# Performance work log

Measured on AMD Instinct MI355X. Metric: run time of the kernel, lower is better.

Reference implementation:

```python
import jax, jax.numpy as jnp
import numpy as np

N = 8192
F_DIM = 512
H_DIM = 256


def _xavier(key, shape):
    fan_in, fan_out = shape
    limit = float(np.sqrt(6.0 / (fan_in + fan_out)))
    return jax.random.uniform(key, shape, jnp.float32, -limit, limit)


def setup_inputs() -> dict:
    key = jax.random.key(0)
    k1, k2, k3, k4, k5, k6, k7 = jax.random.split(key, 7)
    inp = {
        "input": jax.random.normal(k1, (N, F_DIM), jnp.float32),
        "wavelets": jax.random.normal(k2, (N, N), jnp.float32) / np.sqrt(N),
        "wavelets_inv": jax.random.normal(k3, (N, N), jnp.float32) / np.sqrt(N),
        "W1": _xavier(k4, (F_DIM, H_DIM)),
        "W2": _xavier(k5, (H_DIM, H_DIM)),
        "filter1": jax.random.uniform(k6, (N,), jnp.float32, 0.9, 1.1),
        "filter2": jax.random.uniform(k7, (N,), jnp.float32, 0.9, 1.1),
    }
    return inp


def _gwnn_layer(x, wavelets, wavelets_inv, weight, filt):
    # torch: wavelets @ diag(filt) @ (wavelets_inv @ (x @ W))
    # diag(filt) right-multiply == column-wise scale of wavelets (same math,
    # avoids the O(N^3) dense diag matmul).
    t = x @ weight                      # [N, C_out]
    s = wavelets_inv @ t                # [N, C_out] (spectral domain)
    return (wavelets * filt[None, :]) @ s  # [N, C_out]


def reference(input, wavelets, wavelets_inv, W1, W2, filter1, filter2):
    # eval mode: dropout is identity
    h1 = jax.nn.relu(_gwnn_layer(input, wavelets, wavelets_inv, W1, filter1))
    out = _gwnn_layer(h1, wavelets, wavelets_inv, W2, filter2)
    return out
```

## Files before the change

kernel.cpp:

```cpp
#include <hip/hip_runtime.h>
#include <hip/hip_bf16.h>

using f32x4 = __attribute__((ext_vector_type(4))) float;
using s16x8 = __attribute__((ext_vector_type(8))) short;

#define DEVFN static __device__ __forceinline__

static constexpr int NCOL = 256;
static constexpr int MROWS = 8192;
static constexpr int BM = 128;
static constexpr int BK = 64;
static constexpr int THREADS = 512;
static constexpr int NTILE = MROWS / BM;
static constexpr size_t PSLICE = (size_t)MROWS * NCOL;

DEVFN unsigned short f2bf(float f) {
  union { float f; unsigned u; } x; x.f = f;
  unsigned u = x.u;
  u += 0x7fffu + ((u >> 16) & 1u);
  return (unsigned short)(u >> 16);
}

DEVFN float bf2f(unsigned short u) {
  union { unsigned u; float f; } x; x.u = (unsigned)u << 16; return x.f;
}

DEVFN s16x8 pack8(f32x4 v0, f32x4 v1) {
  union { s16x8 v; __hip_bfloat162 h[4]; } pk;
  pk.h[0] = __float22bfloat162_rn(float2{v0[0], v0[1]});
  pk.h[1] = __float22bfloat162_rn(float2{v0[2], v0[3]});
  pk.h[2] = __float22bfloat162_rn(float2{v1[0], v1[1]});
  pk.h[3] = __float22bfloat162_rn(float2{v1[2], v1[3]});
  return pk.v;
}

DEVFN void async16(void* lds, const void* g) {
  __builtin_amdgcn_global_load_lds((const __attribute__((address_space(1))) unsigned*)g,
                                   (__attribute__((address_space(3))) unsigned*)lds,
                                   16, 0, 0);
}


template<int KS>
__global__ __launch_bounds__(THREADS, 2)
void gemm_b(const unsigned short* __restrict__ Ablk, int Kfull,
            const unsigned short* __restrict__ Bp8,
            unsigned short* __restrict__ Pout)
{
  __shared__ __align__(16) unsigned short As[2][2 * 4096];
  __shared__ __align__(16) unsigned short Bs[2][BK * NCOL];

  const int nwg = NTILE * KS, q = nwg / 8;
  const int logical = (blockIdx.x & 7) * q + (blockIdx.x >> 3);
  const int kh = logical / NTILE;
  const int tile = logical % NTILE;
  const int klen = Kfull / KS;
  const int nt = klen / BK;
  const int k0 = kh * klen;
  const int KT = Kfull >> 6;
  const int tid = threadIdx.x, lane = tid & 63;
  const int wm = (tid >> 6) >> 2;
  const int wn = (tid >> 6) & 3;
  const int lr = lane & 15, lg = lane >> 4;

  auto stage = [&](int buf, int t) {
    const unsigned short* asrc = Ablk + ((size_t)(2 * tile) * KT + (k0 >> 6) + t) * 4096 + tid * 8;
    async16(&As[buf][tid * 8], asrc);
    async16(&As[buf][4096 + tid * 8], asrc + (size_t)KT * 4096);
    const unsigned short* bsrc = Bp8 + (size_t)(k0 + t * BK) * NCOL + tid * 8;
#pragma unroll
    for (int o = 0; o < 4; ++o)
      async16(&Bs[buf][o * 4096 + tid * 8], bsrc + o * 4096);
  };

  f32x4 acc[4][4] = {};

  stage(0, 0);

  int cur = 0;
  for (int t = 0; t < nt; ++t) {
    if (t + 1 < nt) {
      stage(cur ^ 1, t + 1);
      asm volatile("s_waitcnt vmcnt(6)");
    } else {
      asm volatile("s_waitcnt vmcnt(0)");
    }
    __builtin_amdgcn_s_barrier();
    __builtin_amdgcn_sched_barrier(0);
#pragma unroll
    for (int s = 0; s < 2; ++s) {
      const int kc = s * 4 + lg;
      s16x8 af[4], bf[4];
#pragma unroll
      for (int fm = 0; fm < 4; ++fm) {
        const int ir = fm * 16 + lr;
        af[fm] = *(const s16x8*)&As[cur][wm * 4096 + ir * 64 + ((kc ^ (ir & 7)) << 3)];
      }
#pragma unroll
      for (int fn = 0; fn < 4; ++fn)
        bf[fn] = *(const s16x8*)&Bs[cur][kc * 2048 + (wn * 64 + fn * 16 + lr) * 8];
#pragma unroll
      for (int fm = 0; fm < 4; ++fm)
#pragma unroll
        for (int fn = 0; fn < 4; ++fn)
          acc[fm][fn] = __builtin_amdgcn_mfma_f32_16x16x32_bf16(af[fm], bf[fn], acc[fm][fn], 0, 0, 0);
    }
    __builtin_amdgcn_s_barrier();
    cur ^= 1;
  }

  unsigned short* dst = Pout + (size_t)kh * PSLICE;
#pragma unroll
  for (int fm = 0; fm < 4; ++fm) {
    const int r0 = tile * BM + wm * 64 + fm * 16 + lg * 4;
#pragma unroll
    for (int fn = 0; fn < 4; ++fn) {
      const int col = wn * 64 + fn * 16 + lr;
      ushort4 u;
      u.x = f2bf(acc[fm][fn][0]); u.y = f2bf(acc[fm][fn][1]);
      u.z = f2bf(acc[fm][fn][2]); u.w = f2bf(acc[fm][fn][3]);
      *(ushort4*)&dst[((size_t)(r0 >> 3) * 256 + col) * 8 + (r0 & 7)] = u;
    }
  }
}


template<int KTSH>
__global__ void k_cvt_ablk(const float* __restrict__ W, unsigned short* __restrict__ outp) {
  const int K = 64 << KTSH;
  size_t gid = (size_t)blockIdx.x * blockDim.x + threadIdx.x;
  const int k8 = (int)(gid & 7);
  const size_t rr = gid >> 3;
  const int row = (int)(rr & 63);
  const size_t bt = rr >> 6;
  const int t = (int)(bt & ((1 << KTSH) - 1));
  const size_t T = bt >> KTSH;
  const float* p = W + (T * 64 + row) * (size_t)K + t * 64 + k8 * 8;
  s16x8 v = pack8(*(const f32x4*)p, *(const f32x4*)(p + 4));
  *(s16x8*)&outp[bt * 4096 + row * 64 + ((k8 ^ (row & 7)) << 3)] = v;
}

__global__ void k_convert_p8(const float* __restrict__ W, int K,
                             unsigned short* __restrict__ outp) {
  int tid = blockIdx.x * blockDim.x + threadIdx.x;
  if (tid >= K * NCOL / 4) return;
  int j = tid & (NCOL - 1);
  int i0 = (tid >> 8) << 2;
  unsigned short u[4];
#pragma unroll
  for (int r = 0; r < 4; ++r) u[r] = f2bf(W[(size_t)(i0 + r) * NCOL + j]);
  size_t off = ((size_t)(i0 >> 3) * NCOL + j) * 8 + (i0 & 7);
  *(ushort4*)&outp[off] = make_ushort4(u[0], u[1], u[2], u[3]);
}

template<int MODE>
__global__ void k_reduce(const unsigned short* __restrict__ P,
                         const float* __restrict__ filt, void* __restrict__ Out) {
  const int tid = blockIdx.x * blockDim.x + threadIdx.x;
  const int j = tid & 255;
  const int i8 = tid >> 8;
  const int i0 = i8 * 8;
  const size_t base = ((size_t)i8 * 256 + j) * 8;
  s16x8 p0 = *(const s16x8*)&P[base];
  s16x8 p1 = *(const s16x8*)&P[base + PSLICE];
  s16x8 p2 = *(const s16x8*)&P[base + 2 * PSLICE];
  s16x8 p3 = *(const s16x8*)&P[base + 3 * PSLICE];
  float f[8];
#pragma unroll
  for (int r = 0; r < 8; ++r)
    f[r] = bf2f((unsigned short)p0[r]) + bf2f((unsigned short)p1[r])
         + bf2f((unsigned short)p2[r]) + bf2f((unsigned short)p3[r]);
  if constexpr (MODE == 0) {
    if (filt) {
#pragma unroll
      for (int r = 0; r < 8; ++r) f[r] *= filt[i0 + r];
    }
    union { s16x8 v; unsigned short u[8]; } o;
#pragma unroll
    for (int r = 0; r < 8; ++r) o.u[r] = f2bf(f[r]);
    *(s16x8*)&((unsigned short*)Out)[base] = o.v;
  } else if constexpr (MODE == 1) {
    unsigned short* O = (unsigned short*)Out;
#pragma unroll
    for (int r = 0; r < 8; ++r) {
      const int row = i0 + r;
      O[((size_t)(row >> 6) * 4 + (j >> 6)) * 4096 + (row & 63) * 64
        + ((((j >> 3) & 7) ^ (row & 7)) << 3) + (j & 7)] = f2bf(fmaxf(f[r], 0.f));
    }
  } else {
    float* O = (float*)Out;
#pragma unroll
    for (int r = 0; r < 8; ++r)
      O[(size_t)(i0 + r) * NCOL + j] = f[r];
  }
}

extern "C" void kernel_launch(void* const* d_in, const int* in_sizes, int n_in,
                              void* d_out, int out_size, void* d_ws, size_t ws_size,
                              hipStream_t stream) {
  const float* input = (const float*)d_in[0];
  const float* Wv    = (const float*)d_in[1];
  const float* Winv  = (const float*)d_in[2];
  const float* W1    = (const float*)d_in[3];
  const float* W2    = (const float*)d_in[4];
  const float* f1    = (const float*)d_in[5];
  const float* f2    = (const float*)d_in[6];
  float* out = (float*)d_out;

  char* ws = (char*)d_ws;
  unsigned short* WvB   = (unsigned short*)(ws);
  unsigned short* WinvB = (unsigned short*)(ws + 0x8000000);
  unsigned short* inB   = (unsigned short*)(ws + 0x10000000);
  unsigned short* partB = (unsigned short*)(ws + 0x10800000);
  unsigned short* t1p   = (unsigned short*)(ws + 0x11800000);
  unsigned short* s1p   = (unsigned short*)(ws + 0x11C00000);
  unsigned short* t2p   = (unsigned short*)(ws + 0x12000000);
  unsigned short* s2p   = (unsigned short*)(ws + 0x12400000);
  unsigned short* h1b   = (unsigned short*)(ws + 0x12800000);
  unsigned short* W1p   = (unsigned short*)(ws + 0x12C00000);
  unsigned short* W2p   = (unsigned short*)(ws + 0x12C40000);

  dim3 gT(THREADS);
  dim3 g4(NTILE * 4), g1(NTILE);
  dim3 rT(256), rG(MROWS * NCOL / 8 / 256);

  k_cvt_ablk<7><<<dim3(32768), rT, 0, stream>>>(Wv, WvB);
  k_cvt_ablk<7><<<dim3(32768), rT, 0, stream>>>(Winv, WinvB);
  k_cvt_ablk<3><<<dim3(2048),  rT, 0, stream>>>(input, inB);
  k_convert_p8<<<dim3(128), rT, 0, stream>>>(W1, 512, W1p);
  k_convert_p8<<<dim3(64),  rT, 0, stream>>>(W2, 256, W2p);

  gemm_b<1><<<g1, gT, 0, stream>>>(inB, 512, W1p, t1p);
  gemm_b<4><<<g4, gT, 0, stream>>>(WinvB, 8192, t1p, partB);
  k_reduce<0><<<rG, rT, 0, stream>>>(partB, f1, s1p);
  gemm_b<4><<<g4, gT, 0, stream>>>(WvB, 8192, s1p, partB);
  k_reduce<1><<<rG, rT, 0, stream>>>(partB, nullptr, h1b);
  gemm_b<1><<<g1, gT, 0, stream>>>(h1b, 256, W2p, t2p);
  gemm_b<4><<<g4, gT, 0, stream>>>(WinvB, 8192, t2p, partB);
  k_reduce<0><<<rG, rT, 0, stream>>>(partB, f2, s2p);
  gemm_b<4><<<g4, gT, 0, stream>>>(WvB, 8192, s2p, partB);
  k_reduce<2><<<rG, rT, 0, stream>>>(partB, nullptr, out);
}
```

Before: 414.0 us.

## Use 256-row tiles with BK=32, 4-stage pipeline and 8-way split-K

Replaces the 128-row, BK=64 double-buffered GEMM with a 256-row tile, BK=32 k-steps and a 4-deep async LDS ring that keeps up to three stages in flight. Split-K goes from 4 to 8 and applies to every GEMM, including the small x@W products, which now also pass through a reduction kernel. The A-operand pre-layout changes to a non-swizzled 256x32 block format. The larger tile raises reuse of the B operand and deeper prefetch hides load latency. In exchange, the partial-sum buffers and reduction traffic double, two extra reduce launches are added, and the unswizzled LDS reads may cause bank conflicts.

```diff
diff --git a/kernel.cpp b/kernel.cpp
--- a/kernel.cpp
+++ b/kernel.cpp
@@ -8,10 +8,9 @@
 
 static constexpr int NCOL = 256;
 static constexpr int MROWS = 8192;
-static constexpr int BM = 128;
-static constexpr int BK = 64;
-static constexpr int THREADS = 512;
-static constexpr int NTILE = MROWS / BM;
+static constexpr int BM = 256;
+static constexpr int KS = 8;
+static constexpr int NT = MROWS / BM;
 static constexpr size_t PSLICE = (size_t)MROWS * NCOL;
 
 DEVFN unsigned short f2bf(float f) {
@@ -41,78 +40,72 @@
 }
 
 
-template<int KS>
-__global__ __launch_bounds__(THREADS, 2)
-void gemm_b(const unsigned short* __restrict__ Ablk, int Kfull,
-            const unsigned short* __restrict__ Bp8,
-            unsigned short* __restrict__ Pout)
+__global__ __launch_bounds__(512, 2)
+void gemm256(const unsigned short* __restrict__ Ap, int Kfull,
+             const unsigned short* __restrict__ Bp8,
+             unsigned short* __restrict__ Pout)
 {
-  __shared__ __align__(16) unsigned short As[2][2 * 4096];
-  __shared__ __align__(16) unsigned short Bs[2][BK * NCOL];
-
-  const int nwg = NTILE * KS, q = nwg / 8;
+  __shared__ __align__(16) unsigned short As[4][8192];
+  __shared__ __align__(16) unsigned short Bs[4][8192];
+
+  const int nwg = NT * KS, q = nwg / 8;
   const int logical = (blockIdx.x & 7) * q + (blockIdx.x >> 3);
-  const int kh = logical / NTILE;
-  const int tile = logical % NTILE;
+  const int kh = logical / NT;
+  const int tile = logical % NT;
   const int klen = Kfull / KS;
-  const int nt = klen / BK;
+  const int nt = klen / 32;
   const int k0 = kh * klen;
-  const int KT = Kfull >> 6;
+  const int KT = Kfull >> 5;
+  const int kt0 = k0 >> 5;
   const int tid = threadIdx.x, lane = tid & 63;
   const int wm = (tid >> 6) >> 2;
   const int wn = (tid >> 6) & 3;
   const int lr = lane & 15, lg = lane >> 4;
 
   auto stage = [&](int buf, int t) {
-    const unsigned short* asrc = Ablk + ((size_t)(2 * tile) * KT + (k0 >> 6) + t) * 4096 + tid * 8;
-    async16(&As[buf][tid * 8], asrc);
-    async16(&As[buf][4096 + tid * 8], asrc + (size_t)KT * 4096);
-    const unsigned short* bsrc = Bp8 + (size_t)(k0 + t * BK) * NCOL + tid * 8;
-#pragma unroll
-    for (int o = 0; o < 4; ++o)
-      async16(&Bs[buf][o * 4096 + tid * 8], bsrc + o * 4096);
+    const unsigned short* a = Ap + ((size_t)tile * KT + kt0 + t) * 8192 + tid * 8;
+    async16(&As[buf][tid * 8], a);
+    async16(&As[buf][4096 + tid * 8], a + 4096);
+    const unsigned short* b = Bp8 + (size_t)(k0 + t * 32) * 256 + tid * 8;
+    async16(&Bs[buf][tid * 8], b);
+    async16(&Bs[buf][4096 + tid * 8], b + 4096);
   };
 
-  f32x4 acc[4][4] = {};
-
-  stage(0, 0);
-
-  int cur = 0;
+  f32x4 acc[8][4] = {};
+
+  if (nt > 0) stage(0, 0);
+  if (nt > 1) stage(1, 1);
+  if (nt > 2) stage(2, 2);
+
   for (int t = 0; t < nt; ++t) {
-    if (t + 1 < nt) {
-      stage(cur ^ 1, t + 1);
-      asm volatile("s_waitcnt vmcnt(6)");
-    } else {
-      asm volatile("s_waitcnt vmcnt(0)");
-    }
+    if (t + 3 < nt) stage((t + 3) & 3, t + 3);
+    const int rem = (nt - 1 - t) < 3 ? (nt - 1 - t) : 3;
+    if (rem == 3)      asm volatile("s_waitcnt vmcnt(12)");
+    else if (rem == 2) asm volatile("s_waitcnt vmcnt(8)");
+    else if (rem == 1) asm volatile("s_waitcnt vmcnt(4)");
+    else               asm volatile("s_waitcnt vmcnt(0)");
     __builtin_amdgcn_s_barrier();
     __builtin_amdgcn_sched_barrier(0);
-#pragma unroll
-    for (int s = 0; s < 2; ++s) {
-      const int kc = s * 4 + lg;
-      s16x8 af[4], bf[4];
-#pragma unroll
-      for (int fm = 0; fm < 4; ++fm) {
-        const int ir = fm * 16 + lr;
-        af[fm] = *(const s16x8*)&As[cur][wm * 4096 + ir * 64 + ((kc ^ (ir & 7)) << 3)];
-      }
+    const int cur = t & 3;
+    s16x8 bfr[4];
+#pragma unroll
+    for (int fn = 0; fn < 4; ++fn)
+      bfr[fn] = *(const s16x8*)&Bs[cur][lg * 2048 + (wn * 64 + fn * 16 + lr) * 8];
+#pragma unroll
+    for (int fm = 0; fm < 8; ++fm) {
+      const int row = wm * 128 + fm * 16 + lr;
+      s16x8 af = *(const s16x8*)&As[cur][lg * 2048 + row * 8];
 #pragma unroll
       for (int fn = 0; fn < 4; ++fn)
-        bf[fn] = *(const s16x8*)&Bs[cur][kc * 2048 + (wn * 64 + fn * 16 + lr) * 8];
-#pragma unroll
-      for (int fm = 0; fm < 4; ++fm)
-#pragma unroll
-        for (int fn = 0; fn < 4; ++fn)
-          acc[fm][fn] = __builtin_amdgcn_mfma_f32_16x16x32_bf16(af[fm], bf[fn], acc[fm][fn], 0, 0, 0);
+        acc[fm][fn] = __builtin_amdgcn_mfma_f32_16x16x32_bf16(af, bfr[fn], acc[fm][fn], 0, 0, 0);
     }
     __builtin_amdgcn_s_barrier();
-    cur ^= 1;
   }
 
   unsigned short* dst = Pout + (size_t)kh * PSLICE;
 #pragma unroll
-  for (int fm = 0; fm < 4; ++fm) {
-    const int r0 = tile * BM + wm * 64 + fm * 16 + lg * 4;
+  for (int fm = 0; fm < 8; ++fm) {
+    const int r0 = tile * BM + wm * 128 + fm * 16 + lg * 4;
 #pragma unroll
     for (int fn = 0; fn < 4; ++fn) {
       const int col = wn * 64 + fn * 16 + lr;
@@ -126,18 +119,16 @@
 
 
 template<int KTSH>
-__global__ void k_cvt_ablk(const float* __restrict__ W, unsigned short* __restrict__ outp) {
-  const int K = 64 << KTSH;
-  size_t gid = (size_t)blockIdx.x * blockDim.x + threadIdx.x;
-  const int k8 = (int)(gid & 7);
-  const size_t rr = gid >> 3;
-  const int row = (int)(rr & 63);
-  const size_t bt = rr >> 6;
-  const int t = (int)(bt & ((1 << KTSH) - 1));
-  const size_t T = bt >> KTSH;
-  const float* p = W + (T * 64 + row) * (size_t)K + t * 64 + k8 * 8;
+__global__ void k_cvt_ap(const float* __restrict__ W, unsigned short* __restrict__ outp) {
+  const int K = 32 << KTSH;
+  const int bt = blockIdx.x;
+  const int kt = bt & ((1 << KTSH) - 1);
+  const int T = bt >> KTSH;
+  const int kc = threadIdx.x >> 8;
+  const int row = threadIdx.x & 255;
+  const float* p = W + ((size_t)T * 256 + row) * K + kt * 32 + kc * 8;
   s16x8 v = pack8(*(const f32x4*)p, *(const f32x4*)(p + 4));
-  *(s16x8*)&outp[bt * 4096 + row * 64 + ((k8 ^ (row & 7)) << 3)] = v;
+  *(s16x8*)&outp[(size_t)bt * 8192 + kc * 2048 + row * 8] = v;
 }
 
 __global__ void k_convert_p8(const float* __restrict__ W, int K,
@@ -161,15 +152,13 @@
   const int i8 = tid >> 8;
   const int i0 = i8 * 8;
   const size_t base = ((size_t)i8 * 256 + j) * 8;
-  s16x8 p0 = *(const s16x8*)&P[base];
-  s16x8 p1 = *(const s16x8*)&P[base + PSLICE];
-  s16x8 p2 = *(const s16x8*)&P[base + 2 * PSLICE];
-  s16x8 p3 = *(const s16x8*)&P[base + 3 * PSLICE];
-  float f[8];
-#pragma unroll
-  for (int r = 0; r < 8; ++r)
-    f[r] = bf2f((unsigned short)p0[r]) + bf2f((unsigned short)p1[r])
-         + bf2f((unsigned short)p2[r]) + bf2f((unsigned short)p3[r]);
+  float f[8] = {};
+#pragma unroll
+  for (int h = 0; h < 8; ++h) {
+    s16x8 pv = *(const s16x8*)&P[base + (size_t)h * PSLICE];
+#pragma unroll
+    for (int r = 0; r < 8; ++r) f[r] += bf2f((unsigned short)pv[r]);
+  }
   if constexpr (MODE == 0) {
     if (filt) {
 #pragma unroll
@@ -184,8 +173,8 @@
 #pragma unroll
     for (int r = 0; r < 8; ++r) {
       const int row = i0 + r;
-      O[((size_t)(row >> 6) * 4 + (j >> 6)) * 4096 + (row & 63) * 64
-        + ((((j >> 3) & 7) ^ (row & 7)) << 3) + (j & 7)] = f2bf(fmaxf(f[r], 0.f));
+      O[((size_t)(row >> 8) * 8 + (j >> 5)) * 8192 + ((j >> 3) & 3) * 2048
+        + (row & 255) * 8 + (j & 7)] = f2bf(fmaxf(f[r], 0.f));
     }
   } else {
     float* O = (float*)Out;
@@ -212,32 +201,34 @@
   unsigned short* WinvB = (unsigned short*)(ws + 0x8000000);
   unsigned short* inB   = (unsigned short*)(ws + 0x10000000);
   unsigned short* partB = (unsigned short*)(ws + 0x10800000);
-  unsigned short* t1p   = (unsigned short*)(ws + 0x11800000);
-  unsigned short* s1p   = (unsigned short*)(ws + 0x11C00000);
-  unsigned short* t2p   = (unsigned short*)(ws + 0x12000000);
-  unsigned short* s2p   = (unsigned short*)(ws + 0x12400000);
-  unsigned short* h1b   = (unsigned short*)(ws + 0x12800000);
-  unsigned short* W1p   = (unsigned short*)(ws + 0x12C00000);
-  unsigned short* W2p   = (unsigned short*)(ws + 0x12C40000);
-
-  dim3 gT(THREADS);
-  dim3 g4(NTILE * 4), g1(NTILE);
+  unsigned short* t1p   = (unsigned short*)(ws + 0x12800000);
+  unsigned short* s1p   = (unsigned short*)(ws + 0x12C00000);
+  unsigned short* t2p   = (unsigned short*)(ws + 0x13000000);
+  unsigned short* s2p   = (unsigned short*)(ws + 0x13400000);
+  unsigned short* h1b   = (unsigned short*)(ws + 0x13800000);
+  unsigned short* W1p   = (unsigned short*)(ws + 0x13C00000);
+  unsigned short* W2p   = (unsigned short*)(ws + 0x13C40000);
+
+  dim3 gemmG(NT * KS), gemmT(512);
+  dim3 cvT(1024);
   dim3 rT(256), rG(MROWS * NCOL / 8 / 256);
 
-  k_cvt_ablk<7><<<dim3(32768), rT, 0, stream>>>(Wv, WvB);
-  k_cvt_ablk<7><<<dim3(32768), rT, 0, stream>>>(Winv, WinvB);
-  k_cvt_ablk<3><<<dim3(2048),  rT, 0, stream>>>(input, inB);
+  k_cvt_ap<8><<<dim3(32 * 256), cvT, 0, stream>>>(Wv, WvB);
+  k_cvt_ap<8><<<dim3(32 * 256), cvT, 0, stream>>>(Winv, WinvB);
+  k_cvt_ap<4><<<dim3(32 * 16),  cvT, 0, stream>>>(input, inB);
   k_convert_p8<<<dim3(128), rT, 0, stream>>>(W1, 512, W1p);
   k_convert_p8<<<dim3(64),  rT, 0, stream>>>(W2, 256, W2p);
 
-  gemm_b<1><<<g1, gT, 0, stream>>>(inB, 512, W1p, t1p);
-  gemm_b<4><<<g4, gT, 0, stream>>>(WinvB, 8192, t1p, partB);
+  gemm256<<<gemmG, gemmT, 0, stream>>>(inB, 512, W1p, partB);
+  k_reduce<0><<<rG, rT, 0, stream>>>(partB, nullptr, t1p);
+  gemm256<<<gemmG, gemmT, 0, stream>>>(WinvB, 8192, t1p, partB);
   k_reduce<0><<<rG, rT, 0, stream>>>(partB, f1, s1p);
-  gemm_b<4><<<g4, gT, 0, stream>>>(WvB, 8192, s1p, partB);
+  gemm256<<<gemmG, gemmT, 0, stream>>>(WvB, 8192, s1p, partB);
   k_reduce<1><<<rG, rT, 0, stream>>>(partB, nullptr, h1b);
-  gemm_b<1><<<g1, gT, 0, stream>>>(h1b, 256, W2p, t2p);
-  gemm_b<4><<<g4, gT, 0, stream>>>(WinvB, 8192, t2p, partB);
+  gemm256<<<gemmG, gemmT, 0, stream>>>(h1b, 256, W2p, partB);
+  k_reduce<0><<<rG, rT, 0, stream>>>(partB, nullptr, t2p);
+  gemm256<<<gemmG, gemmT, 0, stream>>>(WinvB, 8192, t2p, partB);
   k_reduce<0><<<rG, rT, 0, stream>>>(partB, f2, s2p);
-  gemm_b<4><<<g4, gT, 0, stream>>>(WvB, 8192, s2p, partB);
+  gemm256<<<gemmG, gemmT, 0, stream>>>(WvB, 8192, s2p, partB);
   k_reduce<2><<<rG, rT, 0, stream>>>(partB, nullptr, out);
 }
```

Measured after the change: 478.9 us. 1.16x slower.

## Halve GEMM K-tile, raise occupancy, and double split-K with new A layout

Applied to the files above, without the earlier changes.

Reduces the K tile from 64 to 32, shrinking LDS per block so the launch bound allows four blocks per CU instead of two. The split-K factor is doubled (8 for the big GEMMs, 2 for the small ones), and the reduce kernel is templated on the slice count. The A operand gets a new K-major 128x32 blocked layout with no XOR swizzle. This trades more partial-sum traffic (eight bf16 slices to reduce), extra reduce launches for the small GEMMs, and possible LDS bank conflicts for more concurrent workgroups and better latency hiding.

```diff
diff --git a/kernel.cpp b/kernel.cpp
--- a/kernel.cpp
+++ b/kernel.cpp
@@ -9,7 +9,7 @@
 static constexpr int NCOL = 256;
 static constexpr int MROWS = 8192;
 static constexpr int BM = 128;
-static constexpr int BK = 64;
+static constexpr int BK = 32;
 static constexpr int THREADS = 512;
 static constexpr int NTILE = MROWS / BM;
 static constexpr size_t PSLICE = (size_t)MROWS * NCOL;
@@ -42,13 +42,13 @@
 
 
 template<int KS>
-__global__ __launch_bounds__(THREADS, 2)
-void gemm_b(const unsigned short* __restrict__ Ablk, int Kfull,
+__global__ __launch_bounds__(THREADS, 4)
+void gemm_b(const unsigned short* __restrict__ Ap, int Kfull,
             const unsigned short* __restrict__ Bp8,
             unsigned short* __restrict__ Pout)
 {
-  __shared__ __align__(16) unsigned short As[2][2 * 4096];
-  __shared__ __align__(16) unsigned short Bs[2][BK * NCOL];
+  __shared__ __align__(16) unsigned short As[2][4096];
+  __shared__ __align__(16) unsigned short Bs[2][8192];
 
   const int nwg = NTILE * KS, q = nwg / 8;
   const int logical = (blockIdx.x & 7) * q + (blockIdx.x >> 3);
@@ -57,20 +57,18 @@
   const int klen = Kfull / KS;
   const int nt = klen / BK;
   const int k0 = kh * klen;
-  const int KT = Kfull >> 6;
+  const int KT = Kfull >> 5;
+  const int kt0 = k0 >> 5;
   const int tid = threadIdx.x, lane = tid & 63;
   const int wm = (tid >> 6) >> 2;
   const int wn = (tid >> 6) & 3;
   const int lr = lane & 15, lg = lane >> 4;
 
   auto stage = [&](int buf, int t) {
-    const unsigned short* asrc = Ablk + ((size_t)(2 * tile) * KT + (k0 >> 6) + t) * 4096 + tid * 8;
-    async16(&As[buf][tid * 8], asrc);
-    async16(&As[buf][4096 + tid * 8], asrc + (size_t)KT * 4096);
-    const unsigned short* bsrc = Bp8 + (size_t)(k0 + t * BK) * NCOL + tid * 8;
-#pragma unroll
-    for (int o = 0; o < 4; ++o)
-      async16(&Bs[buf][o * 4096 + tid * 8], bsrc + o * 4096);
+    async16(&As[buf][tid * 8], Ap + ((size_t)tile * KT + kt0 + t) * 4096 + tid * 8);
+    const unsigned short* bsrc = Bp8 + (size_t)(k0 + t * BK) * 256 + tid * 8;
+    async16(&Bs[buf][tid * 8], bsrc);
+    async16(&Bs[buf][4096 + tid * 8], bsrc + 4096);
   };
 
   f32x4 acc[4][4] = {};
@@ -81,30 +79,26 @@
   for (int t = 0; t < nt; ++t) {
     if (t + 1 < nt) {
       stage(cur ^ 1, t + 1);
-      asm volatile("s_waitcnt vmcnt(6)");
+      asm volatile("s_waitcnt vmcnt(3)");
     } else {
       asm volatile("s_waitcnt vmcnt(0)");
     }
     __builtin_amdgcn_s_barrier();
     __builtin_amdgcn_sched_barrier(0);
-#pragma unroll
-    for (int s = 0; s < 2; ++s) {
-      const int kc = s * 4 + lg;
-      s16x8 af[4], bf[4];
-#pragma unroll
-      for (int fm = 0; fm < 4; ++fm) {
-        const int ir = fm * 16 + lr;
-        af[fm] = *(const s16x8*)&As[cur][wm * 4096 + ir * 64 + ((kc ^ (ir & 7)) << 3)];
-      }
+    s16x8 af[4], bf[4];
+#pragma unroll
+    for (int fm = 0; fm < 4; ++fm) {
+      const int row = wm * 64 + fm * 16 + lr;
+      af[fm] = *(const s16x8*)&As[cur][lg * 1024 + row * 8];
+    }
+#pragma unroll
+    for (int fn = 0; fn < 4; ++fn)
+      bf[fn] = *(const s16x8*)&Bs[cur][lg * 2048 + (wn * 64 + fn * 16 + lr) * 8];
+#pragma unroll
+    for (int fm = 0; fm < 4; ++fm)
 #pragma unroll
       for (int fn = 0; fn < 4; ++fn)
-        bf[fn] = *(const s16x8*)&Bs[cur][kc * 2048 + (wn * 64 + fn * 16 + lr) * 8];
-#pragma unroll
-      for (int fm = 0; fm < 4; ++fm)
-#pragma unroll
-        for (int fn = 0; fn < 4; ++fn)
-          acc[fm][fn] = __builtin_amdgcn_mfma_f32_16x16x32_bf16(af[fm], bf[fn], acc[fm][fn], 0, 0, 0);
-    }
+        acc[fm][fn] = __builtin_amdgcn_mfma_f32_16x16x32_bf16(af[fm], bf[fn], acc[fm][fn], 0, 0, 0);
     __builtin_amdgcn_s_barrier();
     cur ^= 1;
   }
@@ -126,18 +120,18 @@
 
 
 template<int KTSH>
-__global__ void k_cvt_ablk(const float* __restrict__ W, unsigned short* __restrict__ outp) {
-  const int K = 64 << KTSH;
+__global__ void k_cvt_ap(const float* __restrict__ W, unsigned short* __restrict__ outp) {
+  const int K = 32 << KTSH;
   size_t gid = (size_t)blockIdx.x * blockDim.x + threadIdx.x;
-  const int k8 = (int)(gid & 7);
-  const size_t rr = gid >> 3;
-  const int row = (int)(rr & 63);
-  const size_t bt = rr >> 6;
-  const int t = (int)(bt & ((1 << KTSH) - 1));
+  const int k8 = (int)(gid & 3);
+  const size_t rr = gid >> 2;
+  const int row = (int)(rr & 127);
+  const size_t bt = rr >> 7;
+  const int kt = (int)(bt & ((1 << KTSH) - 1));
   const size_t T = bt >> KTSH;
-  const float* p = W + (T * 64 + row) * (size_t)K + t * 64 + k8 * 8;
+  const float* p = W + (T * 128 + row) * (size_t)K + kt * 32 + k8 * 8;
   s16x8 v = pack8(*(const f32x4*)p, *(const f32x4*)(p + 4));
-  *(s16x8*)&outp[bt * 4096 + row * 64 + ((k8 ^ (row & 7)) << 3)] = v;
+  *(s16x8*)&outp[bt * 4096 + k8 * 1024 + row * 8] = v;
 }
 
 __global__ void k_convert_p8(const float* __restrict__ W, int K,
@@ -153,7 +147,7 @@
   *(ushort4*)&outp[off] = make_ushort4(u[0], u[1], u[2], u[3]);
 }
 
-template<int MODE>
+template<int NS, int MODE>
 __global__ void k_reduce(const unsigned short* __restrict__ P,
                          const float* __restrict__ filt, void* __restrict__ Out) {
   const int tid = blockIdx.x * blockDim.x + threadIdx.x;
@@ -161,15 +155,13 @@
   const int i8 = tid >> 8;
   const int i0 = i8 * 8;
   const size_t base = ((size_t)i8 * 256 + j) * 8;
-  s16x8 p0 = *(const s16x8*)&P[base];
-  s16x8 p1 = *(const s16x8*)&P[base + PSLICE];
-  s16x8 p2 = *(const s16x8*)&P[base + 2 * PSLICE];
-  s16x8 p3 = *(const s16x8*)&P[base + 3 * PSLICE];
-  float f[8];
-#pragma unroll
-  for (int r = 0; r < 8; ++r)
-    f[r] = bf2f((unsigned short)p0[r]) + bf2f((unsigned short)p1[r])
-         + bf2f((unsigned short)p2[r]) + bf2f((unsigned short)p3[r]);
+  float f[8] = {};
+#pragma unroll
+  for (int h = 0; h < NS; ++h) {
+    s16x8 pv = *(const s16x8*)&P[base + (size_t)h * PSLICE];
+#pragma unroll
+    for (int r = 0; r < 8; ++r) f[r] += bf2f((unsigned short)pv[r]);
+  }
   if constexpr (MODE == 0) {
     if (filt) {
 #pragma unroll
@@ -184,8 +176,8 @@
 #pragma unroll
     for (int r = 0; r < 8; ++r) {
       const int row = i0 + r;
-      O[((size_t)(row >> 6) * 4 + (j >> 6)) * 4096 + (row & 63) * 64
-        + ((((j >> 3) & 7) ^ (row & 7)) << 3) + (j & 7)] = f2bf(fmaxf(f[r], 0.f));
+      O[((size_t)(row >> 7) * 8 + (j >> 5)) * 4096 + ((j >> 3) & 3) * 1024
+        + (row & 127) * 8 + (j & 7)] = f2bf(fmaxf(f[r], 0.f));
     }
   } else {
     float* O = (float*)Out;
@@ -212,32 +204,34 @@
   unsigned short* WinvB = (unsigned short*)(ws + 0x8000000);
   unsigned short* inB   = (unsigned short*)(ws + 0x10000000);
   unsigned short* partB = (unsigned short*)(ws + 0x10800000);
-  unsigned short* t1p   = (unsigned short*)(ws + 0x11800000);
-  unsigned short* s1p   = (unsigned short*)(ws + 0x11C00000);
-  unsigned short* t2p   = (unsigned short*)(ws + 0x12000000);
-  unsigned short* s2p   = (unsigned short*)(ws + 0x12400000);
-  unsigned short* h1b   = (unsigned short*)(ws + 0x12800000);
-  unsigned short* W1p   = (unsigned short*)(ws + 0x12C00000);
-  unsigned short* W2p   = (unsigned short*)(ws + 0x12C40000);
+  unsigned short* t1p   = (unsigned short*)(ws + 0x12800000);
+  unsigned short* s1p   = (unsigned short*)(ws + 0x12C00000);
+  unsigned short* t2p   = (unsigned short*)(ws + 0x13000000);
+  unsigned short* s2p   = (unsigned short*)(ws + 0x13400000);
+  unsigned short* h1b   = (unsigned short*)(ws + 0x13800000);
+  unsigned short* W1p   = (unsigned short*)(ws + 0x13C00000);
+  unsigned short* W2p   = (unsigned short*)(ws + 0x13C40000);
 
   dim3 gT(THREADS);
-  dim3 g4(NTILE * 4), g1(NTILE);
+  dim3 g8(NTILE * 8), g2(NTILE * 2);
   dim3 rT(256), rG(MROWS * NCOL / 8 / 256);
 
-  k_cvt_ablk<7><<<dim3(32768), rT, 0, stream>>>(Wv, WvB);
-  k_cvt_ablk<7><<<dim3(32768), rT, 0, stream>>>(Winv, WinvB);
-  k_cvt_ablk<3><<<dim3(2048),  rT, 0, stream>>>(input, inB);
+  k_cvt_ap<8><<<dim3(32768), rT, 0, stream>>>(Wv, WvB);
+  k_cvt_ap<8><<<dim3(32768), rT, 0, stream>>>(Winv, WinvB);
+  k_cvt_ap<4><<<dim3(2048),  rT, 0, stream>>>(input, inB);
   k_convert_p8<<<dim3(128), rT, 0, stream>>>(W1, 512, W1p);
   k_convert_p8<<<dim3(64),  rT, 0, stream>>>(W2, 256, W2p);
 
-  gemm_b<1><<<g1, gT, 0, stream>>>(inB, 512, W1p, t1p);
-  gemm_b<4><<<g4, gT, 0, stream>>>(WinvB, 8192, t1p, partB);
-  k_reduce<0><<<rG, rT, 0, stream>>>(partB, f1, s1p);
-  gemm_b<4><<<g4, gT, 0, stream>>>(WvB, 8192, s1p, partB);
-  k_reduce<1><<<rG, rT, 0, stream>>>(partB, nullptr, h1b);
-  gemm_b<1><<<g1, gT, 0, stream>>>(h1b, 256, W2p, t2p);
-  gemm_b<4><<<g4, gT, 0, stream>>>(WinvB, 8192, t2p, partB);
-  k_reduce<0><<<rG, rT, 0, stream>>>(partB, f2, s2p);
-  gemm_b<4><<<g4, gT, 0, stream>>>(WvB, 8192, s2p, partB);
-  k_reduce<2><<<rG, rT, 0, stream>>>(partB, nullptr, out);
-}
+  gemm_b<2><<<g2, gT, 0, stream>>>(inB, 512, W1p, partB);
+  k_reduce<2, 0><<<rG, rT, 0, stream>>>(partB, nullptr, t1p);
+  gemm_b<8><<<g8, gT, 0, stream>>>(WinvB, 8192, t1p, partB);
+  k_reduce<8, 0><<<rG, rT, 0, stream>>>(partB, f1, s1p);
+  gemm_b<8><<<g8, gT, 0, stream>>>(WvB, 8192, s1p, partB);
+  k_reduce<8, 1><<<rG, rT, 0, stream>>>(partB, nullptr, h1b);
+  gemm_b<2><<<g2, gT, 0, stream>>>(h1b, 256, W2p, partB);
+  k_reduce<2, 0><<<rG, rT, 0, stream>>>(partB, nullptr, t2p);
+  gemm_b<8><<<g8, gT, 0, stream>>>(WinvB, 8192, t2p, partB);
+  k_reduce<8, 0><<<rG, rT, 0, stream>>>(partB, f2, s2p);
+  gemm_b<8><<<g8, gT, 0, stream>>>(WvB, 8192, s2p, partB);
+  k_reduce<8, 2><<<rG, rT, 0, stream>>>(partB, nullptr, out);
+}
```

Result: faster. 397.8 us (-3.9%).
